# Optimization experiments

Measured on AMD Instinct MI355X. Metric: run time of the kernel, lower is better.

The kernel has to match this reference:

```python
import jax, jax.numpy as jnp
import numpy as np

B, S, D, UNITS = 64, 2048, 512, 256

def setup_inputs() -> dict:
    key = jax.random.key(0)
    ks = jax.random.split(key, 8)
    sd = 1.0 / np.sqrt(D)
    query = jax.random.normal(ks[0], (B, D), dtype=jnp.float32)
    values = jax.random.normal(ks[1], (B, S, D), dtype=jnp.float32)
    W1 = jax.random.normal(ks[2], (D, UNITS), dtype=jnp.float32) * sd
    b1 = jnp.zeros((UNITS,), dtype=jnp.float32)
    W2 = jax.random.normal(ks[3], (D, UNITS), dtype=jnp.float32) * sd
    b2 = jnp.zeros((UNITS,), dtype=jnp.float32)
    V = jax.random.normal(ks[4], (UNITS, 1), dtype=jnp.float32) * (1.0 / np.sqrt(UNITS))
    bV = jnp.zeros((1,), dtype=jnp.float32)
    return {"query": query, "values": values, "W1": W1, "b1": b1,
            "W2": W2, "b2": b2, "V": V, "bV": bV}

def reference(query, values, W1, b1, W2, b2, V, bV):
    # proj_v: [B, S, U]; proj_q: [B, 1, U]
    proj_v = jnp.einsum('bsd,du->bsu', values, W1) + b1
    proj_q = (query @ W2 + b2)[:, None, :]
    # score: [B, S, 1]
    score = jnp.tanh(proj_v + proj_q) @ V + bV
    attn = jax.nn.softmax(score, axis=1)           # softmax over sequence axis
    context = jnp.sum(attn * values, axis=1)        # [B, D]
    return context
```

## Files before the change

kernel.cpp:

```cpp
#include <hip/hip_runtime.h>
#include <hip/hip_bf16.h>

typedef unsigned short u16;
typedef unsigned int u32;
typedef __attribute__((ext_vector_type(8))) short short8;
typedef __attribute__((ext_vector_type(4))) float f32x4;

#define NB 64
#define NS 2048
#define ND 512
#define NU 256
#define CH 32
#define CPB (NS / CH)
#define ASTR 520

__device__ __forceinline__ u16 f2b(float f) {
    u32 x = __float_as_uint(f);
    u32 r = (x + 0x7FFFu + ((x >> 16) & 1u)) >> 16;
    return (u16)r;
}
__device__ __forceinline__ u32 pk2(float lo, float hi) {
    __hip_bfloat162 h = __float22bfloat162_rn(float2{lo, hi});
    return *(u32*)&h;
}
__device__ __forceinline__ float fast_tanh(float x) {
    float e = __expf(2.0f * x);
    return 1.0f - 2.0f / (e + 1.0f);
}

__global__ __launch_bounds__(256) void cbias_kernel(
    const float* __restrict__ q, const float* __restrict__ W2,
    const float* __restrict__ b1, const float* __restrict__ b2,
    float* __restrict__ cb)
{
    int b = blockIdx.x, u = threadIdx.x;
    __shared__ float qs[ND];
    qs[u]       = q[b * ND + u];
    qs[u + 256] = q[b * ND + u + 256];
    __syncthreads();
    float acc = 0.f;
#pragma unroll 8
    for (int d = 0; d < ND; d++)
        acc += qs[d] * W2[d * NU + u];
    cb[b * NU + u] = acc + b1[u] + b2[u];
}

__global__ __launch_bounds__(256) void transpose_kernel(
    const float* __restrict__ W1, u16* __restrict__ W1Tc)
{
    __shared__ float tile[64][65];
    int k0 = blockIdx.x * 64;
    int u0 = blockIdx.y * 64;
    for (int i = threadIdx.x; i < 4096; i += 256) {
        int r = i >> 6, c = i & 63;
        tile[r][c] = W1[(k0 + r) * NU + u0 + c];
    }
    __syncthreads();
    for (int i = threadIdx.x; i < 4096; i += 256) {
        int r = i >> 6, c = i & 63;
        W1Tc[blockIdx.x * (NU * 64) + (u0 + r) * 64 + c] = f2b(tile[c][r]);
    }
}

__global__ __launch_bounds__(256, 4) void fused_kernel(
    const float* __restrict__ values,
    const u16* __restrict__ W1Tc,
    const float* __restrict__ cb,
    const float* __restrict__ V,
    float* __restrict__ ctxp,
    float2* __restrict__ meta)
{
    const int tid  = threadIdx.x;
    const int lane = tid & 63;
    const int wn   = tid >> 6;
    const int m16  = lane & 15;
    const int quad = lane >> 4;

    const int mblk = blockIdx.x;
    const int b    = mblk >> 6;
    const size_t base_row = (size_t)mblk * CH;

    __shared__ u16 Afull[CH][ASTR];
    __shared__ float cbs[NU];
    __shared__ float Vs[NU];
    __shared__ float rowsum[CH];
    __shared__ float wsm[CH];
    __shared__ float mred[2];

    cbs[tid] = cb[b * NU + tid];
    Vs[tid]  = V[tid];
    if (tid < CH) rowsum[tid] = 0.f;

    f32x4 acc[2][4] = {};

    const int arow = tid >> 3, acol = (tid & 7) * 8;
    const float* asrc = values + (base_row + arow) * ND + acol;

    float4 v0 = ((const float4*)asrc)[0];
    float4 v1 = ((const float4*)asrc)[1];

    for (int kc = 0; kc < 8; kc++) {
        {
            uint4 q0;
            q0.x = pk2(v0.x, v0.y); q0.y = pk2(v0.z, v0.w);
            q0.z = pk2(v1.x, v1.y); q0.w = pk2(v1.z, v1.w);
            *(uint4*)&Afull[arow][kc * 64 + acol] = q0;
        }
        __syncthreads();
        if (kc < 7) {
            const float* nsrc = asrc + (kc + 1) * 64;
            v0 = ((const float4*)nsrc)[0];
            v1 = ((const float4*)nsrc)[1];
        }
        short8 bfr[2][4];
#pragma unroll
        for (int kh = 0; kh < 2; kh++)
#pragma unroll
            for (int cbk = 0; cbk < 4; cbk++)
                bfr[kh][cbk] = *(const short8*)(W1Tc + (size_t)kc * (NU * 64)
                                + (wn * 64 + cbk * 16 + m16) * 64 + kh * 32 + quad * 8);
#pragma unroll
        for (int kh = 0; kh < 2; kh++) {
            short8 afr[2];
#pragma unroll
            for (int rb = 0; rb < 2; rb++)
                afr[rb] = *(const short8*)&Afull[rb * 16 + m16][kc * 64 + kh * 32 + quad * 8];
#pragma unroll
            for (int rb = 0; rb < 2; rb++)
#pragma unroll
                for (int cbk = 0; cbk < 4; cbk++)
                    acc[rb][cbk] = __builtin_amdgcn_mfma_f32_16x16x32_bf16(
                        afr[rb], bfr[kh][cbk], acc[rb][cbk], 0, 0, 0);
        }
    }

    float cbv[4], vv[4];
#pragma unroll
    for (int cbk = 0; cbk < 4; cbk++) {
        int c = wn * 64 + cbk * 16 + m16;
        cbv[cbk] = cbs[c];
        vv[cbk]  = Vs[c];
    }
#pragma unroll
    for (int rb = 0; rb < 2; rb++) {
#pragma unroll
        for (int i = 0; i < 4; i++) {
            float s = 0.f;
#pragma unroll
            for (int cbk = 0; cbk < 4; cbk++)
                s += fast_tanh(acc[rb][cbk][i] + cbv[cbk]) * vv[cbk];
            s += __shfl_xor(s, 1, 64);
            s += __shfl_xor(s, 2, 64);
            s += __shfl_xor(s, 4, 64);
            s += __shfl_xor(s, 8, 64);
            if (m16 == 0)
                atomicAdd(&rowsum[rb * 16 + quad * 4 + i], s);
        }
    }
    __syncthreads();

    if (tid < CH) {
        float s = rowsum[tid];
        float m = s;
        m = fmaxf(m, __shfl_xor(m, 1, 64));
        m = fmaxf(m, __shfl_xor(m, 2, 64));
        m = fmaxf(m, __shfl_xor(m, 4, 64));
        m = fmaxf(m, __shfl_xor(m, 8, 64));
        m = fmaxf(m, __shfl_xor(m, 16, 64));
        float w = __expf(s - m);
        wsm[tid] = w;
        float l = w;
        l += __shfl_xor(l, 1, 64);
        l += __shfl_xor(l, 2, 64);
        l += __shfl_xor(l, 4, 64);
        l += __shfl_xor(l, 8, 64);
        l += __shfl_xor(l, 16, 64);
        if (tid == 0) { mred[0] = m; mred[1] = l; }
    }
    __syncthreads();

    {
        const u32* adw = (const u32*)&Afull[0][0];
        float a0 = 0.f, a1 = 0.f;
#pragma unroll 8
        for (int r = 0; r < CH; r++) {
            u32 pk = adw[r * (ASTR / 2) + tid];
            float lo = __uint_as_float(pk << 16);
            float hi = __uint_as_float(pk & 0xFFFF0000u);
            float wt = wsm[r];
            a0 += wt * lo;
            a1 += wt * hi;
        }
        float2* dst = (float2*)(ctxp + (size_t)mblk * ND + tid * 2);
        *dst = float2{a0, a1};
    }
    if (tid == 0) meta[mblk] = float2{mred[0], mred[1]};
}

__global__ __launch_bounds__(256) void combine_kernel(
    const float* __restrict__ ctxp, const float2* __restrict__ meta,
    float* __restrict__ out)
{
    int b = blockIdx.x, tid = threadIdx.x;
    __shared__ float wc[CPB];
    __shared__ float Ls;
    if (tid < CPB) {
        float2 mt = meta[b * CPB + tid];
        float m = mt.x;
        m = fmaxf(m, __shfl_xor(m, 1, 64));
        m = fmaxf(m, __shfl_xor(m, 2, 64));
        m = fmaxf(m, __shfl_xor(m, 4, 64));
        m = fmaxf(m, __shfl_xor(m, 8, 64));
        m = fmaxf(m, __shfl_xor(m, 16, 64));
        m = fmaxf(m, __shfl_xor(m, 32, 64));
        float w = __expf(mt.x - m);
        wc[tid] = w;
        float l = w * mt.y;
        l += __shfl_xor(l, 1, 64);
        l += __shfl_xor(l, 2, 64);
        l += __shfl_xor(l, 4, 64);
        l += __shfl_xor(l, 8, 64);
        l += __shfl_xor(l, 16, 64);
        l += __shfl_xor(l, 32, 64);
        if (tid == 0) Ls = l;
    }
    __syncthreads();
    float inv = 1.0f / Ls;
    float s0 = 0.f, s1 = 0.f;
#pragma unroll 4
    for (int c = 0; c < CPB; c++) {
        const float* p = ctxp + ((size_t)b * CPB + c) * ND;
        float w = wc[c];
        s0 += w * p[tid];
        s1 += w * p[tid + 256];
    }
    out[b * ND + tid]       = s0 * inv;
    out[b * ND + tid + 256] = s1 * inv;
}

extern "C" void kernel_launch(void* const* d_in, const int* in_sizes, int n_in,
                              void* d_out, int out_size, void* d_ws, size_t ws_size,
                              hipStream_t stream)
{
    const float* q      = (const float*)d_in[0];
    const float* values = (const float*)d_in[1];
    const float* W1     = (const float*)d_in[2];
    const float* b1     = (const float*)d_in[3];
    const float* W2     = (const float*)d_in[4];
    const float* b2     = (const float*)d_in[5];
    const float* V      = (const float*)d_in[6];

    char* ws = (char*)d_ws;
    float*  cb    = (float*) (ws);
    u16*    W1Tc  = (u16*)   (ws + 65536);
    float*  ctxp  = (float*) (ws + 327680);
    float2* meta  = (float2*)(ws + 327680 + 8388608);

    hipLaunchKernelGGL(cbias_kernel, dim3(64), dim3(256), 0, stream, q, W2, b1, b2, cb);
    hipLaunchKernelGGL(transpose_kernel, dim3(8, 4), dim3(256), 0, stream, W1, W1Tc);
    hipLaunchKernelGGL(fused_kernel, dim3(NB * CPB), dim3(256), 0, stream,
                       values, W1Tc, cb, V, ctxp, meta);
    hipLaunchKernelGGL(combine_kernel, dim3(64), dim3(256), 0, stream,
                       ctxp, meta, (float*)d_out);
}
```

Baseline: 498.2 us.

## Double chunk size, prestage A tile, fragment-order W1 with double-buffered B loads

Raises the rows handled per block from 32 to 64, so each W1 fragment loaded from global memory feeds twice as many MFMAs and half as many partial contexts are written. The whole 64x512 values tile is converted into LDS up front, which removes the per-k-chunk barrier. W1 is prepacked into MFMA fragment order so each lane's B load is contiguous, and B fragments for the next chunk are prefetched into a second register buffer. The two prep kernels are merged into one launch, and the row-score LDS atomics are replaced by per-wave partial sums. In exchange, the larger LDS tile and register footprint lower occupancy (launch bounds go from 4 to 2 blocks per SM) and the grid has half as many blocks.

```diff
diff --git a/kernel.cpp b/kernel.cpp
--- a/kernel.cpp
+++ b/kernel.cpp
@@ -10,7 +10,7 @@
 #define NS 2048
 #define ND 512
 #define NU 256
-#define CH 32
+#define CH 64
 #define CPB (NS / CH)
 #define ASTR 520
 
@@ -28,43 +28,46 @@
     return 1.0f - 2.0f / (e + 1.0f);
 }
 
-__global__ __launch_bounds__(256) void cbias_kernel(
+__global__ __launch_bounds__(256) void prep_kernel(
     const float* __restrict__ q, const float* __restrict__ W2,
     const float* __restrict__ b1, const float* __restrict__ b2,
-    float* __restrict__ cb)
-{
-    int b = blockIdx.x, u = threadIdx.x;
-    __shared__ float qs[ND];
-    qs[u]       = q[b * ND + u];
-    qs[u + 256] = q[b * ND + u + 256];
-    __syncthreads();
-    float acc = 0.f;
+    const float* __restrict__ W1,
+    float* __restrict__ cb, u16* __restrict__ W1Tf)
+{
+    const int tid = threadIdx.x;
+    if (blockIdx.x < 64) {
+        int b = blockIdx.x, u = tid;
+        __shared__ float qs[ND];
+        qs[u]       = q[b * ND + u];
+        qs[u + 256] = q[b * ND + u + 256];
+        __syncthreads();
+        float acc = 0.f;
 #pragma unroll 8
-    for (int d = 0; d < ND; d++)
-        acc += qs[d] * W2[d * NU + u];
-    cb[b * NU + u] = acc + b1[u] + b2[u];
-}
-
-__global__ __launch_bounds__(256) void transpose_kernel(
-    const float* __restrict__ W1, u16* __restrict__ W1Tc)
-{
-    __shared__ float tile[64][65];
-    int k0 = blockIdx.x * 64;
-    int u0 = blockIdx.y * 64;
-    for (int i = threadIdx.x; i < 4096; i += 256) {
-        int r = i >> 6, c = i & 63;
-        tile[r][c] = W1[(k0 + r) * NU + u0 + c];
-    }
-    __syncthreads();
-    for (int i = threadIdx.x; i < 4096; i += 256) {
-        int r = i >> 6, c = i & 63;
-        W1Tc[blockIdx.x * (NU * 64) + (u0 + r) * 64 + c] = f2b(tile[c][r]);
-    }
-}
-
-__global__ __launch_bounds__(256, 4) void fused_kernel(
+        for (int d = 0; d < ND; d++)
+            acc += qs[d] * W2[d * NU + u];
+        cb[b * NU + u] = acc + b1[u] + b2[u];
+    } else {
+        int blk = blockIdx.x - 64;
+#pragma unroll
+        for (int it = 0; it < 8; it++) {
+            int id   = blk * 2048 + it * 256 + tid;
+            int f    = id >> 6, lane = id & 63;
+            int cbk  = f & 3, kh = (f >> 2) & 1, wn = (f >> 3) & 3, kc = f >> 5;
+            int m16  = lane & 15, quad = lane >> 4;
+            int u    = wn * 64 + cbk * 16 + m16;
+            int kb   = kc * 64 + kh * 32 + quad * 8;
+            u16 tmp[8];
+#pragma unroll
+            for (int j = 0; j < 8; j++)
+                tmp[j] = f2b(W1[(kb + j) * NU + u]);
+            *(uint4*)&W1Tf[(size_t)id * 8] = *(uint4*)tmp;
+        }
+    }
+}
+
+__global__ __launch_bounds__(256, 2) void fused_kernel(
     const float* __restrict__ values,
-    const u16* __restrict__ W1Tc,
+    const u16* __restrict__ W1Tf,
     const float* __restrict__ cb,
     const float* __restrict__ V,
     float* __restrict__ ctxp,
@@ -77,61 +80,74 @@
     const int quad = lane >> 4;
 
     const int mblk = blockIdx.x;
-    const int b    = mblk >> 6;
+    const int b    = mblk >> 5;
     const size_t base_row = (size_t)mblk * CH;
 
     __shared__ u16 Afull[CH][ASTR];
     __shared__ float cbs[NU];
     __shared__ float Vs[NU];
-    __shared__ float rowsum[CH];
+    __shared__ float rsum4[4][CH];
     __shared__ float wsm[CH];
     __shared__ float mred[2];
 
     cbs[tid] = cb[b * NU + tid];
     Vs[tid]  = V[tid];
-    if (tid < CH) rowsum[tid] = 0.f;
-
-    f32x4 acc[2][4] = {};
-
-    const int arow = tid >> 3, acol = (tid & 7) * 8;
-    const float* asrc = values + (base_row + arow) * ND + acol;
-
-    float4 v0 = ((const float4*)asrc)[0];
-    float4 v1 = ((const float4*)asrc)[1];
-
+
+    const int arow = tid >> 2;
+    const int acol = (tid & 3) * 16;
+    const float* asrc = values + (base_row + arow) * ND + (tid & 3) * 16;
+#pragma unroll
+    for (int h = 0; h < 2; h++) {
+        float4 v[4][4];
+#pragma unroll
+        for (int k4 = 0; k4 < 4; k4++)
+#pragma unroll
+            for (int j = 0; j < 4; j++)
+                v[k4][j] = ((const float4*)(asrc + (h * 4 + k4) * 64))[j];
+#pragma unroll
+        for (int k4 = 0; k4 < 4; k4++) {
+            int kc = h * 4 + k4;
+            uint4 q0, q1;
+            q0.x = pk2(v[k4][0].x, v[k4][0].y); q0.y = pk2(v[k4][0].z, v[k4][0].w);
+            q0.z = pk2(v[k4][1].x, v[k4][1].y); q0.w = pk2(v[k4][1].z, v[k4][1].w);
+            q1.x = pk2(v[k4][2].x, v[k4][2].y); q1.y = pk2(v[k4][2].z, v[k4][2].w);
+            q1.z = pk2(v[k4][3].x, v[k4][3].y); q1.w = pk2(v[k4][3].z, v[k4][3].w);
+            *(uint4*)&Afull[arow][kc * 64 + acol]     = q0;
+            *(uint4*)&Afull[arow][kc * 64 + acol + 8] = q1;
+        }
+    }
+    __syncthreads();
+
+    f32x4 acc[4][4] = {};
+    const u16* pB = W1Tf + wn * 4096 + lane * 8;
+
+    short8 bfr[2][8];
+#pragma unroll
+    for (int f = 0; f < 8; f++)
+        bfr[0][f] = *(const short8*)(pB + f * 512);
+
+#pragma unroll
     for (int kc = 0; kc < 8; kc++) {
-        {
-            uint4 q0;
-            q0.x = pk2(v0.x, v0.y); q0.y = pk2(v0.z, v0.w);
-            q0.z = pk2(v1.x, v1.y); q0.w = pk2(v1.z, v1.w);
-            *(uint4*)&Afull[arow][kc * 64 + acol] = q0;
-        }
-        __syncthreads();
+        const int cur = kc & 1, nxt = cur ^ 1;
         if (kc < 7) {
-            const float* nsrc = asrc + (kc + 1) * 64;
-            v0 = ((const float4*)nsrc)[0];
-            v1 = ((const float4*)nsrc)[1];
-        }
-        short8 bfr[2][4];
+#pragma unroll
+            for (int f = 0; f < 8; f++)
+                bfr[nxt][f] = *(const short8*)(pB + (kc + 1) * 16384 + f * 512);
+        }
+        short8 afr[2][4];
 #pragma unroll
         for (int kh = 0; kh < 2; kh++)
 #pragma unroll
-            for (int cbk = 0; cbk < 4; cbk++)
-                bfr[kh][cbk] = *(const short8*)(W1Tc + (size_t)kc * (NU * 64)
-                                + (wn * 64 + cbk * 16 + m16) * 64 + kh * 32 + quad * 8);
-#pragma unroll
-        for (int kh = 0; kh < 2; kh++) {
-            short8 afr[2];
-#pragma unroll
-            for (int rb = 0; rb < 2; rb++)
-                afr[rb] = *(const short8*)&Afull[rb * 16 + m16][kc * 64 + kh * 32 + quad * 8];
-#pragma unroll
-            for (int rb = 0; rb < 2; rb++)
+            for (int rb = 0; rb < 4; rb++)
+                afr[kh][rb] = *(const short8*)&Afull[rb * 16 + m16][kc * 64 + kh * 32 + quad * 8];
+#pragma unroll
+        for (int kh = 0; kh < 2; kh++)
+#pragma unroll
+            for (int rb = 0; rb < 4; rb++)
 #pragma unroll
                 for (int cbk = 0; cbk < 4; cbk++)
                     acc[rb][cbk] = __builtin_amdgcn_mfma_f32_16x16x32_bf16(
-                        afr[rb], bfr[kh][cbk], acc[rb][cbk], 0, 0, 0);
-        }
+                        afr[kh][rb], bfr[cur][kh * 4 + cbk], acc[rb][cbk], 0, 0, 0);
     }
 
     float cbv[4], vv[4];
@@ -142,7 +158,7 @@
         vv[cbk]  = Vs[c];
     }
 #pragma unroll
-    for (int rb = 0; rb < 2; rb++) {
+    for (int rb = 0; rb < 4; rb++) {
 #pragma unroll
         for (int i = 0; i < 4; i++) {
             float s = 0.f;
@@ -154,19 +170,20 @@
             s += __shfl_xor(s, 4, 64);
             s += __shfl_xor(s, 8, 64);
             if (m16 == 0)
-                atomicAdd(&rowsum[rb * 16 + quad * 4 + i], s);
+                rsum4[wn][rb * 16 + quad * 4 + i] = s;
         }
     }
     __syncthreads();
 
     if (tid < CH) {
-        float s = rowsum[tid];
+        float s = rsum4[0][tid] + rsum4[1][tid] + rsum4[2][tid] + rsum4[3][tid];
         float m = s;
         m = fmaxf(m, __shfl_xor(m, 1, 64));
         m = fmaxf(m, __shfl_xor(m, 2, 64));
         m = fmaxf(m, __shfl_xor(m, 4, 64));
         m = fmaxf(m, __shfl_xor(m, 8, 64));
         m = fmaxf(m, __shfl_xor(m, 16, 64));
+        m = fmaxf(m, __shfl_xor(m, 32, 64));
         float w = __expf(s - m);
         wsm[tid] = w;
         float l = w;
@@ -175,6 +192,7 @@
         l += __shfl_xor(l, 4, 64);
         l += __shfl_xor(l, 8, 64);
         l += __shfl_xor(l, 16, 64);
+        l += __shfl_xor(l, 32, 64);
         if (tid == 0) { mred[0] = m; mred[1] = l; }
     }
     __syncthreads();
@@ -212,7 +230,6 @@
         m = fmaxf(m, __shfl_xor(m, 4, 64));
         m = fmaxf(m, __shfl_xor(m, 8, 64));
         m = fmaxf(m, __shfl_xor(m, 16, 64));
-        m = fmaxf(m, __shfl_xor(m, 32, 64));
         float w = __expf(mt.x - m);
         wc[tid] = w;
         float l = w * mt.y;
@@ -221,7 +238,6 @@
         l += __shfl_xor(l, 4, 64);
         l += __shfl_xor(l, 8, 64);
         l += __shfl_xor(l, 16, 64);
-        l += __shfl_xor(l, 32, 64);
         if (tid == 0) Ls = l;
     }
     __syncthreads();
@@ -252,14 +268,14 @@
 
     char* ws = (char*)d_ws;
     float*  cb    = (float*) (ws);
-    u16*    W1Tc  = (u16*)   (ws + 65536);
+    u16*    W1Tf  = (u16*)   (ws + 65536);
     float*  ctxp  = (float*) (ws + 327680);
-    float2* meta  = (float2*)(ws + 327680 + 8388608);
-
-    hipLaunchKernelGGL(cbias_kernel, dim3(64), dim3(256), 0, stream, q, W2, b1, b2, cb);
-    hipLaunchKernelGGL(transpose_kernel, dim3(8, 4), dim3(256), 0, stream, W1, W1Tc);
+    float2* meta  = (float2*)(ws + 327680 + 4194304);
+
+    hipLaunchKernelGGL(prep_kernel, dim3(72), dim3(256), 0, stream,
+                       q, W2, b1, b2, W1, cb, W1Tf);
     hipLaunchKernelGGL(fused_kernel, dim3(NB * CPB), dim3(256), 0, stream,
-                       values, W1Tc, cb, V, ctxp, meta);
+                       values, W1Tf, cb, V, ctxp, meta);
     hipLaunchKernelGGL(combine_kernel, dim3(64), dim3(256), 0, stream,
                        ctxp, meta, (float*)d_out);
 }
```

New measurement: 445.4 us. 1.12x faster.
